# Kernel optimization log

Hardware: AMD Instinct MI355X
Metric: run time of the kernel (lower is better)

Reference implementation:

```python
import jax, jax.numpy as jnp
import numpy as np

B, M, L = 100, 100, 8
N = M * L
EPS = 1e-5  # torch BatchNorm2d default eps


def _conv(x, w, b, stride, pad):
    y = jax.lax.conv_general_dilated(x, w, (stride, stride), [(pad, pad), (pad, pad)],
                                     dimension_numbers=('NCHW', 'OIHW', 'NCHW'))
    return y + b[None, :, None, None]


def _convT(x, w, b, stride, pad):
    # torch ConvTranspose2d weight layout: (in_ch, out_ch, kH, kW)
    k = w.shape[2]
    wt = jnp.flip(w, (2, 3)).transpose(1, 0, 2, 3)  # -> OIHW
    p = k - 1 - pad
    y = jax.lax.conv_general_dilated(x, wt, (1, 1), [(p, p), (p, p)],
                                     lhs_dilation=(stride, stride),
                                     dimension_numbers=('NCHW', 'OIHW', 'NCHW'))
    return y + b[None, :, None, None]


def _bn(x):
    # BatchNorm2d constructed fresh in forward: weight=1, bias=0, batch stats (biased var)
    mean = x.mean(axis=(0, 2, 3), keepdims=True)
    var = x.var(axis=(0, 2, 3), keepdims=True)
    return (x - mean) / jnp.sqrt(var + EPS)


def _leaky(x):
    return jnp.where(x >= 0, x, 0.01 * x)


def _forward(x, conv1_w, conv1_b, conv2_w, conv2_b, conv3_w, conv3_b, conv4_w, conv4_b,
             fc_w, fc_b, dec_w, dec_b, ct1_w, ct1_b, ct2_w, ct2_b, ct3_w, ct3_b,
             ct4_w, ct4_b, ct5_w, ct5_b):
    # ---- encoder ----
    h = _bn(_leaky(_conv(x, conv1_w, conv1_b, 2, 1)))   # (B,128,32,32)
    h = _bn(_leaky(_conv(h, conv2_w, conv2_b, 2, 1)))   # (B,256,16,16)
    h = _bn(_leaky(_conv(h, conv3_w, conv3_b, 2, 1)))   # (B,1024,8,8)
    h = _bn(_leaky(_conv(h, conv4_w, conv4_b, 2, 1)))   # (B,1024,4,4)
    eig = jax.nn.relu(h.reshape(B, -1) @ fc_w + fc_b)   # (B, 800)
    # ---- latent_sample (training branch) ----
    sig = eig.reshape(B, M, L)
    row = jnp.sqrt(float(M * L)) * jnp.fft.ifft2(sig)          # complex (B,M,L)
    # original builds C via numpy/scipy per-sample -> detached; circulant[i,j] = c[(i-j) % n]
    row_flat = jax.lax.stop_gradient(row.real.reshape(B, N))
    i = jnp.arange(N)
    idx = (i[:, None] - i[None, :]) % N                        # (N,N) circulant gather
    C = row_flat[:, idx]                                       # (B,N,N)
    # original: Sigma_batch_eps[:, i] = eigenvalue (noise zeta is dead code), via numpy -> detached
    Y = jnp.fft.fft2(jax.lax.stop_gradient(sig)).real          # (B,M,L)
    # ---- decoder ----
    d = (Y.reshape(B, N) @ dec_w + dec_b).reshape(B, 1024, 3, 3)
    d = _convT(d, ct1_w, ct1_b, 2, 1)   # (B,512,5,5)
    d = _convT(d, ct2_w, ct2_b, 2, 0)   # (B,256,11,11)
    d = _convT(d, ct3_w, ct3_b, 2, 0)   # (B,128,23,23)
    d = _convT(d, ct4_w, ct4_b, 2, 0)   # (B,64,47,47)
    d = _convT(d, ct5_w, ct5_b, 1, 0)   # (B,1,49,49)
    return d, C, eig


def setup_inputs():
    key = jax.random.key(0)
    ks = jax.random.split(key, 16)

    def wv(k, shape, fan_in):
        return (jax.random.normal(k, shape, jnp.float32) / np.sqrt(fan_in)).astype(jnp.float32)

    return {
        'x': jax.random.normal(ks[0], (B, 1, 64, 64), jnp.float32),
        'conv1_w': wv(ks[1], (128, 1, 3, 3), 9), 'conv1_b': jnp.zeros((128,), jnp.float32),
        'conv2_w': wv(ks[2], (256, 128, 3, 3), 128 * 9), 'conv2_b': jnp.zeros((256,), jnp.float32),
        'conv3_w': wv(ks[3], (1024, 256, 3, 3), 256 * 9), 'conv3_b': jnp.zeros((1024,), jnp.float32),
        'conv4_w': wv(ks[4], (1024, 1024, 3, 3), 1024 * 9), 'conv4_b': jnp.zeros((1024,), jnp.float32),
        'fc_w': wv(ks[5], (1024 * 16, N), 1024 * 16), 'fc_b': jnp.zeros((N,), jnp.float32),
        'dec_w': wv(ks[6], (N, 1024 * 9), N), 'dec_b': jnp.zeros((1024 * 9,), jnp.float32),
        'ct1_w': wv(ks[7], (1024, 512, 3, 3), 1024 * 9), 'ct1_b': jnp.zeros((512,), jnp.float32),
        'ct2_w': wv(ks[8], (512, 256, 3, 3), 512 * 9), 'ct2_b': jnp.zeros((256,), jnp.float32),
        'ct3_w': wv(ks[9], (256, 128, 3, 3), 256 * 9), 'ct3_b': jnp.zeros((128,), jnp.float32),
        'ct4_w': wv(ks[10], (128, 64, 3, 3), 128 * 9), 'ct4_b': jnp.zeros((64,), jnp.float32),
        'ct5_w': wv(ks[11], (64, 1, 3, 3), 64 * 9), 'ct5_b': jnp.zeros((1,), jnp.float32),
    }


def reference(x, conv1_w, conv1_b, conv2_w, conv2_b, conv3_w, conv3_b, conv4_w, conv4_b,
              fc_w, fc_b, dec_w, dec_b, ct1_w, ct1_b, ct2_w, ct2_b, ct3_w, ct3_b,
              ct4_w, ct4_b, ct5_w, ct5_b):
    return _forward(x, conv1_w, conv1_b, conv2_w, conv2_b, conv3_w, conv3_b, conv4_w, conv4_b,
                    fc_w, fc_b, dec_w, dec_b, ct1_w, ct1_b, ct2_w, ct2_b, ct3_w, ct3_b,
                    ct4_w, ct4_b, ct5_w, ct5_b)
```

## Files before the change

kernel.cpp:

```cpp
#include <hip/hip_runtime.h>
#include <math.h>

typedef __attribute__((ext_vector_type(8))) short bf16x8;
typedef __attribute__((ext_vector_type(4))) float f32x4;
typedef unsigned short u16;

__device__ __forceinline__ u16 f2bf(float f) {
    unsigned u = __builtin_bit_cast(unsigned, f);
    u += 0x7FFFu + ((u >> 16) & 1u);
    return (u16)(u >> 16);
}
__device__ __forceinline__ float bf2f(u16 h) {
    unsigned u = ((unsigned)h) << 16;
    return __builtin_bit_cast(float, u);
}

template<int MODE, int OUT, int BM, int BN, int SWIZ, bool STATS>
__global__ __launch_bounds__(256, 3)
void gemm(const u16* __restrict__ Abf, const u16* __restrict__ Bw,
          const float* __restrict__ bias, void* __restrict__ outv,
          float* __restrict__ stat,
          int M, int N, int K, int lgC,
          int IH, int IW, int OH, int OW, int zchunk)
{
    constexpr int ANSEG = BM / 64, BNSEG = BN / 64;
    constexpr int RM = BM / 32, RN = BN / 32;
    __shared__ __align__(16) u16 As[4 * BM * 8];
    __shared__ __align__(16) u16 Bs[4 * BN * 8];
    const int t = threadIdx.x;
    const int lane = t & 63, wave = t >> 6;
    const int lm = lane & 15, quad = lane >> 4;
    const int wm = wave & 1, wn = wave >> 1;
    int mt, nt, z;
    if (SWIZ == 1) {
        int mtN = (M + BM - 1) / BM;
        int id = blockIdx.x;
        nt = id & 7; int j = id >> 3;
        mt = j % mtN; z = j / mtN;
    } else { mt = blockIdx.x; nt = blockIdx.y; z = blockIdx.z; }
    const int k0 = z * zchunk, kend = k0 + zchunk;

    const int arow = (ANSEG == 2) ? (t >> 1) : (t >> 2);
    const int akb  = (ANSEG == 2) ? (t & 1) * 16 : (t & 3) * 8;
    const int a_gm = mt * BM + arow;
    const bool a_in = a_gm < M;
    int oy = 0, ox = 0, bimg = 0;
    if (MODE == 1) {
        int ohw = OH * OW;
        int g = a_in ? a_gm : 0;
        bimg = g / ohw; int r = g - bimg * ohw;
        oy = r / OW; ox = r - (r / OW) * OW;
    }
    const int brow = (BNSEG == 2) ? (t >> 1) : (t >> 2);
    const int bkb  = (BNSEG == 2) ? (t & 1) * 16 : (t & 3) * 8;
    const int b_gn = nt * BN + brow;
    const bool b_in = b_gn < N;

    f32x4 acc[RM][RN];
    #pragma unroll
    for (int i = 0; i < RM; i++)
        #pragma unroll
        for (int j = 0; j < RN; j++) acc[i][j] = (f32x4){0.f, 0.f, 0.f, 0.f};

    for (int kb = k0; kb < kend; kb += 32) {
        #pragma unroll
        for (int s = 0; s < ANSEG; s++) {
            int kk = kb + akb + s * 8;
            uint4 v = make_uint4(0, 0, 0, 0);
            if (MODE == 0) {
                if (a_in) v = *(const uint4*)(Abf + (size_t)a_gm * K + kk);
            } else {
                int tap = kk >> lgC;
                int ic = kk & ((1 << lgC) - 1);
                int ky = tap / 3, kx = tap - (tap / 3) * 3;
                int iy = oy * 2 - 1 + ky, ix = ox * 2 - 1 + kx;
                if (a_in && (unsigned)iy < (unsigned)IH && (unsigned)ix < (unsigned)IW)
                    v = *(const uint4*)(Abf + ((((size_t)bimg * IH + iy) * IW + ix) << lgC) + ic);
            }
            *(uint4*)&As[(((akb >> 3) + s) * BM + arow) * 8] = v;
        }
        #pragma unroll
        for (int s = 0; s < BNSEG; s++) {
            int kk = kb + bkb + s * 8;
            uint4 v = make_uint4(0, 0, 0, 0);
            if (b_in) v = *(const uint4*)(Bw + (size_t)b_gn * K + kk);
            *(uint4*)&Bs[(((bkb >> 3) + s) * BN + brow) * 8] = v;
        }
        __syncthreads();
        bf16x8 af[RM], bfr[RN];
        #pragma unroll
        for (int i = 0; i < RM; i++)
            af[i] = *(const bf16x8*)&As[(size_t)(quad * BM + wm * (BM / 2) + i * 16 + lm) * 8];
        #pragma unroll
        for (int j = 0; j < RN; j++)
            bfr[j] = *(const bf16x8*)&Bs[(size_t)(quad * BN + wn * (BN / 2) + j * 16 + lm) * 8];
        #pragma unroll
        for (int i = 0; i < RM; i++)
            #pragma unroll
            for (int j = 0; j < RN; j++)
                acc[i][j] = __builtin_amdgcn_mfma_f32_16x16x32_bf16(af[i], bfr[j], acc[i][j], 0, 0, 0);
        __syncthreads();
    }

    const int n_base = nt * BN + wn * (BN / 2);
    const int m_base = mt * BM + wm * (BM / 2);
    int nj[RN]; float bvj[RN];
    #pragma unroll
    for (int j = 0; j < RN; j++) {
        nj[j] = n_base + j * 16 + lm;
        bvj[j] = 0.f;
        if (nj[j] < N && OUT != 4) {
            if (OUT == 0 || OUT == 5) bvj[j] = bias[nj[j]];
            else if (z == 0) bvj[j] = bias[nj[j]];
        }
    }
    if constexpr (OUT == 4) {
        float* op = (float*)outv;
        #pragma unroll
        for (int i = 0; i < RM; i++)
            #pragma unroll
            for (int r = 0; r < 4; r++) {
                int m = m_base + i * 16 + quad * 4 + r;
                if (m >= M) continue;
                #pragma unroll
                for (int j = 0; j < RN; j++)
                    if (nj[j] < N) atomicAdd(&op[(size_t)m * N + nj[j]], acc[i][j][r]);
            }
    } else if constexpr (OUT == 5) {
        u16* op = (u16*)outv;
        #pragma unroll
        for (int j = 0; j < RN; j++) {
            if (nj[j] >= N) continue;
            int c = nj[j] / 9, hw = nj[j] - c * 9;
            #pragma unroll
            for (int i = 0; i < RM; i++)
                #pragma unroll
                for (int r = 0; r < 4; r++) {
                    int m = m_base + i * 16 + quad * 4 + r;
                    if (m >= M) continue;
                    op[((size_t)m * 9 + hw) * 1024 + c] = f2bf(acc[i][j][r] + bvj[j]);
                }
        }
    } else if constexpr (OUT == 0) {
        int ohw = OH * OW;
        float sj[RN], qj[RN];
        #pragma unroll
        for (int j = 0; j < RN; j++) { sj[j] = 0.f; qj[j] = 0.f; }
        #pragma unroll
        for (int i = 0; i < RM; i++) {
            int m0 = m_base + i * 16 + quad * 4;
            if (m0 >= M) continue;
            int b = m0 / ohw, pix = m0 - b * ohw;
            #pragma unroll
            for (int j = 0; j < RN; j++) {
                if (nj[j] >= N) continue;
                #pragma unroll
                for (int r = 0; r < 4; r++) {
                    float val = acc[i][j][r] + bvj[j];
                    ((u16*)outv)[((size_t)b * ohw + pix + r) * N + nj[j]] = f2bf(val);
                    if (STATS) {
                        float lv = val >= 0.f ? val : 0.01f * val;
                        sj[j] += lv; qj[j] += lv * lv;
                    }
                }
            }
        }
        if constexpr (STATS) {
            #pragma unroll
            for (int j = 0; j < RN; j++) {
                float s = sj[j], q = qj[j];
                s += __shfl_down(s, 32); q += __shfl_down(q, 32);
                s += __shfl_down(s, 16); q += __shfl_down(q, 16);
                if (quad == 0 && nj[j] < N) {
                    atomicAdd(&stat[nj[j]], s);
                    atomicAdd(&stat[N + nj[j]], q);
                }
            }
        }
    } else {
        int ohw = OH * OW;
        #pragma unroll
        for (int i = 0; i < RM; i++) {
            int m0 = m_base + i * 16 + quad * 4;
            if (m0 >= M) continue;
            int b = m0 / ohw, pix = m0 - b * ohw;
            #pragma unroll
            for (int j = 0; j < RN; j++) {
                if (nj[j] >= N) continue;
                #pragma unroll
                for (int r = 0; r < 4; r++)
                    atomicAdd(&((float*)outv)[((size_t)b * ohw + pix + r) * N + nj[j]],
                              acc[i][j][r] + bvj[j]);
            }
        }
    }
}

template<int BM>
__global__ __launch_bounds__(256, 3)
void gemm_ct(const u16* __restrict__ Abf, const u16* __restrict__ Wb,
             const float* __restrict__ bias, u16* __restrict__ out,
             int N, int lgC, int IH, int IW, int OH, int OW,
             int4 Kc, int4 Mc, int4 Hc, int4 Wc, int4 Oc, int4 Dy, int4 Dx)
{
    constexpr int ANSEG = BM / 64;
    constexpr int RM = BM / 32, RN = 2;
    const int c = blockIdx.z;
    const int Ks[4] = {Kc.x, Kc.y, Kc.z, Kc.w};
    const int Ms[4] = {Mc.x, Mc.y, Mc.z, Mc.w};
    const int Hs[4] = {Hc.x, Hc.y, Hc.z, Hc.w};
    const int Wsz[4]= {Wc.x, Wc.y, Wc.z, Wc.w};
    const int Os[4] = {Oc.x, Oc.y, Oc.z, Oc.w};
    const int Dys[4]= {Dy.x, Dy.y, Dy.z, Dy.w};
    const int Dxs[4]= {Dx.x, Dx.y, Dx.z, Dx.w};
    const int K = Ks[c], M = Ms[c], OHc = Hs[c], OWc = Wsz[c];
    const int dyp = Dys[c], dxp = Dxs[c];
    const int mt = blockIdx.x, nt = blockIdx.y;
    if (mt * BM >= M) return;
    const u16* Bw = Wb + Os[c];

    __shared__ __align__(16) u16 As[4 * BM * 8];
    __shared__ __align__(16) u16 Bs[4 * 64 * 8];
    const int t = threadIdx.x;
    const int lane = t & 63, wave = t >> 6;
    const int lm = lane & 15, quad = lane >> 4;
    const int wm = wave & 1, wn = wave >> 1;

    const int arow = (ANSEG == 2) ? (t >> 1) : (t >> 2);
    const int akb  = (ANSEG == 2) ? (t & 1) * 16 : (t & 3) * 8;
    const int a_gm = mt * BM + arow;
    const bool a_in = a_gm < M;
    const int ohwc = OHc * OWc;
    int g = a_in ? a_gm : 0;
    int bimg = g / ohwc; int rr = g - bimg * ohwc;
    int oy = rr / OWc, ox = rr - (rr / OWc) * OWc;

    const int brow = t >> 2;
    const int bkb  = (t & 3) * 8;
    const int b_gn = nt * 64 + brow;
    const bool b_in = b_gn < N;

    f32x4 acc[RM][RN];
    #pragma unroll
    for (int i = 0; i < RM; i++)
        #pragma unroll
        for (int j = 0; j < RN; j++) acc[i][j] = (f32x4){0.f, 0.f, 0.f, 0.f};

    for (int kb = 0; kb < K; kb += 32) {
        #pragma unroll
        for (int s = 0; s < ANSEG; s++) {
            int kk = kb + akb + s * 8;
            uint4 v = make_uint4(0, 0, 0, 0);
            int ti = kk >> lgC;
            int ic = kk & ((1 << lgC) - 1);
            int dy = (int)(signed char)((dyp >> (8 * ti)) & 255);
            int dx = (int)(signed char)((dxp >> (8 * ti)) & 255);
            int iy = oy + dy, ix = ox + dx;
            if (a_in && (unsigned)iy < (unsigned)IH && (unsigned)ix < (unsigned)IW)
                v = *(const uint4*)(Abf + ((((size_t)bimg * IH + iy) * IW + ix) << lgC) + ic);
            *(uint4*)&As[(((akb >> 3) + s) * BM + arow) * 8] = v;
        }
        {
            uint4 v = make_uint4(0, 0, 0, 0);
            if (b_in) v = *(const uint4*)(Bw + (size_t)b_gn * K + kb + bkb);
            *(uint4*)&Bs[((bkb >> 3) * 64 + brow) * 8] = v;
        }
        __syncthreads();
        bf16x8 af[RM], bfr[RN];
        #pragma unroll
        for (int i = 0; i < RM; i++)
            af[i] = *(const bf16x8*)&As[(size_t)(quad * BM + wm * (BM / 2) + i * 16 + lm) * 8];
        #pragma unroll
        for (int j = 0; j < RN; j++)
            bfr[j] = *(const bf16x8*)&Bs[(size_t)(quad * 64 + wn * 32 + j * 16 + lm) * 8];
        #pragma unroll
        for (int i = 0; i < RM; i++)
            #pragma unroll
            for (int j = 0; j < RN; j++)
                acc[i][j] = __builtin_amdgcn_mfma_f32_16x16x32_bf16(af[i], bfr[j], acc[i][j], 0, 0, 0);
        __syncthreads();
    }

    const int n_base = nt * 64 + wn * 32;
    const int m_base = mt * BM + wm * (BM / 2);
    const int cy = c >> 1, cx = c & 1;
    const int OHW = OH * OW;
    int nj[RN]; float bvj[RN];
    #pragma unroll
    for (int j = 0; j < RN; j++) {
        nj[j] = n_base + j * 16 + lm;
        bvj[j] = (nj[j] < N) ? bias[nj[j]] : 0.f;
    }
    #pragma unroll
    for (int i = 0; i < RM; i++)
        #pragma unroll
        for (int r = 0; r < 4; r++) {
            int m = m_base + i * 16 + quad * 4 + r;
            if (m >= M) continue;
            int b = m / ohwc, r2 = m - b * ohwc;
            int oyc = r2 / OWc, oxc = r2 - (r2 / OWc) * OWc;
            size_t ad0 = ((size_t)b * OHW + (2 * oyc + cy) * OW + 2 * oxc + cx) * N;
            #pragma unroll
            for (int j = 0; j < RN; j++)
                if (nj[j] < N) out[ad0 + nj[j]] = f2bf(acc[i][j][r] + bvj[j]);
        }
}

__global__ __launch_bounds__(256)
void convw_prep(const float* __restrict__ src, u16* __restrict__ dst, int lgC, int total) {
    int idx = blockIdx.x * 256 + threadIdx.x;
    if (idx >= total) return;
    int K = 9 << lgC;
    int oc = idx / K, kk = idx - oc * K;
    int tap = kk >> lgC, ic = kk & ((1 << lgC) - 1);
    dst[idx] = f2bf(src[(((size_t)oc << lgC) + ic) * 9 + tap]);
}

__global__ __launch_bounds__(256)
void transpose_cvt(const float* __restrict__ in, u16* __restrict__ out, int R, int C) {
    __shared__ float tl[32][33];
    int c0 = blockIdx.x * 32, r0 = blockIdx.y * 32;
    int tx = threadIdx.x & 31, ty = threadIdx.x >> 5;
    #pragma unroll
    for (int l = 0; l < 4; l++)
        tl[ty + 8 * l][tx] = in[(size_t)(r0 + ty + 8 * l) * C + c0 + tx];
    __syncthreads();
    #pragma unroll
    for (int l = 0; l < 4; l++)
        out[(size_t)(c0 + ty + 8 * l) * R + r0 + tx] = f2bf(tl[tx][ty + 8 * l]);
}

__global__ __launch_bounds__(256)
void ctw_gather(const u16* __restrict__ tmp, u16* __restrict__ outw,
                int CIN, int lgC, int OC, int P) {
    int idx = blockIdx.x * 256 + threadIdx.x;
    if (idx >= (OC << lgC)) return;
    int ic = idx & (CIN - 1);
    int oc = idx >> lgC;
    int off = 0;
    for (int c = 0; c < 4; c++) {
        int cyP = (c >> 1) + P, cxP = (c & 1) + P;
        int nky = ((cyP & 1) == 0) ? 2 : 1;
        int nkx = ((cxP & 1) == 0) ? 2 : 1;
        int T = nky * nkx;
        int ti = 0;
        for (int ky = 0; ky < 3; ky++) {
            if ((cyP + ky) & 1) continue;
            for (int kx = 0; kx < 3; kx++) {
                if ((cxP + kx) & 1) continue;
                outw[off + (size_t)oc * (CIN * T) + ti * CIN + ic] =
                    tmp[((size_t)oc * 9 + ky * 3 + kx) * CIN + ic];
                ti++;
            }
        }
        off += OC * CIN * T;
    }
}

__global__ __launch_bounds__(256)
void fcw_prep(const float* __restrict__ in, u16* __restrict__ out) {
    __shared__ float tl[32][33];
    int n0 = blockIdx.x * 32, c0 = blockIdx.y * 32, hw = blockIdx.z;
    int tx = threadIdx.x & 31, ty = threadIdx.x >> 5;
    #pragma unroll
    for (int l = 0; l < 4; l++)
        tl[ty + 8 * l][tx] = in[((size_t)(c0 + ty + 8 * l) * 16 + hw) * 800 + n0 + tx];
    __syncthreads();
    #pragma unroll
    for (int l = 0; l < 4; l++)
        out[(size_t)(n0 + ty + 8 * l) * 16384 + hw * 1024 + c0 + tx] = f2bf(tl[tx][ty + 8 * l]);
}

__global__ __launch_bounds__(256)
void wt5_prep(const float* __restrict__ in, u16* __restrict__ out) {
    int idx = blockIdx.x * 256 + threadIdx.x;
    if (idx >= 576) return;
    int tap = idx >> 6, ic = idx & 63;
    out[idx] = f2bf(in[ic * 9 + tap]);
}

__global__ __launch_bounds__(256)
void conv1_nhwc(const float* __restrict__ x, const float* __restrict__ w,
                const float* __restrict__ bias, u16* __restrict__ out) {
    int idx = blockIdx.x * 256 + threadIdx.x;
    if (idx >= 100 * 1024 * 128) return;
    int oc = idx & 127;
    int pix = (idx >> 7) & 1023;
    int b = idx >> 17;
    int oy = pix >> 5, ox = pix & 31;
    int iy0 = oy * 2 - 1, ix0 = ox * 2 - 1;
    float acc = bias[oc];
    const float* ip = x + (size_t)b * 4096;
    const float* wp = w + oc * 9;
    #pragma unroll
    for (int ky = 0; ky < 3; ky++) {
        int iy = iy0 + ky;
        if ((unsigned)iy >= 64u) continue;
        #pragma unroll
        for (int kx = 0; kx < 3; kx++) {
            int ix = ix0 + kx;
            if ((unsigned)ix >= 64u) continue;
            acc = fmaf(ip[iy * 64 + ix], wp[ky * 3 + kx], acc);
        }
    }
    out[idx] = f2bf(acc);
}

template<typename T>
__global__ __launch_bounds__(256)
void bnstat(const T* __restrict__ x, float* __restrict__ accum, int C, int total) {
    int idx0 = blockIdx.x * 256 + threadIdx.x;
    int stride = gridDim.x * 256;
    float s = 0.f, q = 0.f;
    for (int i = idx0; i < total; i += stride) {
        float v;
        if constexpr (sizeof(T) == 2) v = bf2f(x[i]); else v = x[i];
        v = v >= 0.f ? v : 0.01f * v;
        s += v; q += v * v;
    }
    int c = idx0 & (C - 1);
    atomicAdd(&accum[c], s);
    atomicAdd(&accum[C + c], q);
}

template<typename T>
__global__ __launch_bounds__(256)
void bnapply(const T* __restrict__ x, u16* __restrict__ out,
             const float* __restrict__ accum, int C, int total, float invcnt) {
    int idx = blockIdx.x * 256 + threadIdx.x;
    if (idx >= total) return;
    int c = idx & (C - 1);
    float mean = accum[c] * invcnt;
    float var = accum[C + c] * invcnt - mean * mean;
    float inv = rsqrtf(var + 1e-5f);
    float v;
    if constexpr (sizeof(T) == 2) v = bf2f(x[idx]); else v = x[idx];
    v = v >= 0.f ? v : 0.01f * v;
    out[idx] = f2bf((v - mean) * inv);
}

__global__ __launch_bounds__(256)
void finalize_relu(const float* __restrict__ acc, const float* __restrict__ bias,
                   float* __restrict__ out) {
    int i = blockIdx.x * 256 + threadIdx.x;
    if (i >= 100 * 800) return;
    float v = acc[i] + bias[i % 800];
    out[i] = fmaxf(v, 0.f);
}

__global__ __launch_bounds__(256)
void dft_real(const float* __restrict__ eig, float* __restrict__ Yr, u16* __restrict__ Yrb) {
    __shared__ float se[800];
    __shared__ float ctab[800];
    int b = blockIdx.x;
    for (int i = threadIdx.x; i < 800; i += 256) {
        se[i] = eig[b * 800 + i];
        ctab[i] = (float)cos(6.283185307179586 * (double)i / 800.0);
    }
    __syncthreads();
    for (int oi = threadIdx.x; oi < 800; oi += 256) {
        int k1 = oi >> 3, k2 = oi & 7;
        int d1 = k1 * 8, d2 = k2 * 100;
        float acc = 0.f;
        int p1 = 0;
        for (int n1 = 0; n1 < 100; n1++) {
            int p = p1;
            #pragma unroll
            for (int n2 = 0; n2 < 8; n2++) {
                acc = fmaf(se[n1 * 8 + n2], ctab[p], acc);
                p += d2; if (p >= 800) p -= 800;
            }
            p1 += d1; if (p1 >= 800) p1 -= 800;
        }
        Yr[b * 800 + oi] = acc;
        Yrb[b * 800 + oi] = f2bf(acc);
    }
}

__global__ __launch_bounds__(256)
void build_C4(const float* __restrict__ Yr, float* __restrict__ C) {
    int idx = blockIdx.x * 256 + threadIdx.x;
    if (idx >= 100 * 800 * 200) return;
    int j4 = (idx % 200) * 4; int tt = idx / 200;
    int i = tt % 800;         int b = tt / 800;
    const float* y = Yr + b * 800;
    f32x4 v;
    #pragma unroll
    for (int r = 0; r < 4; r++) {
        int k = i - (j4 + r);
        k += (k >> 31) & 800;
        v[r] = y[k] * 0.035355339059327376f;
    }
    ((f32x4*)C)[idx] = v;
}

__global__ __launch_bounds__(256)
void convT5(const u16* __restrict__ in, const u16* __restrict__ w,
            const float* __restrict__ bias, float* __restrict__ out) {
    int idx = blockIdx.x * 256 + threadIdx.x;
    if (idx >= 100 * 49 * 49) return;
    int ox = idx % 49; int t2 = idx / 49;
    int oy = t2 % 49;  int b = t2 / 49;
    float acc = bias[0];
    for (int ky = 0; ky < 3; ky++) {
        int iy = oy - ky;
        if ((unsigned)iy >= 47u) continue;
        for (int kx = 0; kx < 3; kx++) {
            int ix = ox - kx;
            if ((unsigned)ix >= 47u) continue;
            const uint4* ip = (const uint4*)(in + (((size_t)b * 47 + iy) * 47 + ix) * 64);
            const uint4* wp = (const uint4*)(w + (ky * 3 + kx) * 64);
            #pragma unroll
            for (int g = 0; g < 8; g++) {
                uint4 av = ip[g], wv = wp[g];
                const unsigned* aa = (const unsigned*)&av;
                const unsigned* ww = (const unsigned*)&wv;
                #pragma unroll
                for (int h = 0; h < 4; h++) {
                    float a0 = __builtin_bit_cast(float, aa[h] << 16);
                    float a1 = __builtin_bit_cast(float, aa[h] & 0xFFFF0000u);
                    float w0 = __builtin_bit_cast(float, ww[h] << 16);
                    float w1 = __builtin_bit_cast(float, ww[h] & 0xFFFF0000u);
                    acc = fmaf(a0, w0, acc);
                    acc = fmaf(a1, w1, acc);
                }
            }
        }
    }
    out[idx] = acc;
}

struct CTClass { int T, OHc, OWc, dyp, dxp, off, K; };
static void ct_params(int P, int OH, int OW, int CIN, int OC, CTClass cls[4]) {
    int off = 0;
    for (int c = 0; c < 4; c++) {
        int cy = c >> 1, cx = c & 1;
        int kys[2], dys[2], nky = 0, kxs[2], dxs[2], nkx = 0;
        for (int ky = 0; ky < 3; ky++)
            if (((cy + P + ky) & 1) == 0) { kys[nky] = ky; dys[nky] = (cy + P - ky) / 2; nky++; }
        for (int kx = 0; kx < 3; kx++)
            if (((cx + P + kx) & 1) == 0) { kxs[nkx] = kx; dxs[nkx] = (cx + P - kx) / 2; nkx++; }
        CTClass& cc = cls[c];
        cc.T = nky * nkx;
        cc.OHc = (OH - cy + 1) >> 1; cc.OWc = (OW - cx + 1) >> 1;
        cc.dyp = 0; cc.dxp = 0;
        int ti = 0;
        for (int a = 0; a < nky; a++)
            for (int b2 = 0; b2 < nkx; b2++, ti++) {
                cc.dyp |= (dys[a] & 255) << (8 * ti);
                cc.dxp |= (dxs[b2] & 255) << (8 * ti);
            }
        cc.off = off; cc.K = CIN * cc.T;
        off += OC * cc.K;
    }
}

template<int BM>
static void launch_ct(hipStream_t s, const u16* in, const u16* W, const float* bias, u16* outp,
                      int lgC, int OC, int IH, int IW, int OH, int OW, const CTClass* cls) {
    int maxMT = 0;
    for (int c = 0; c < 4; c++) {
        int mt = (100 * cls[c].OHc * cls[c].OWc + BM - 1) / BM;
        if (mt > maxMT) maxMT = mt;
    }
    dim3 g(maxMT, (OC + 63) / 64, 4);
    gemm_ct<BM><<<g, 256, 0, s>>>(in, W, bias, outp, OC, lgC, IH, IW, OH, OW,
        make_int4(cls[0].K, cls[1].K, cls[2].K, cls[3].K),
        make_int4(100*cls[0].OHc*cls[0].OWc, 100*cls[1].OHc*cls[1].OWc,
                  100*cls[2].OHc*cls[2].OWc, 100*cls[3].OHc*cls[3].OWc),
        make_int4(cls[0].OHc, cls[1].OHc, cls[2].OHc, cls[3].OHc),
        make_int4(cls[0].OWc, cls[1].OWc, cls[2].OWc, cls[3].OWc),
        make_int4(cls[0].off, cls[1].off, cls[2].off, cls[3].off),
        make_int4(cls[0].dyp, cls[1].dyp, cls[2].dyp, cls[3].dyp),
        make_int4(cls[0].dxp, cls[1].dxp, cls[2].dxp, cls[3].dxp));
}

extern "C" void kernel_launch(void* const* d_in, const int* in_sizes, int n_in,
                              void* d_out, int out_size, void* d_ws, size_t ws_size,
                              hipStream_t stream) {
    const float* x    = (const float*)d_in[0];
    const float* c1w  = (const float*)d_in[1];  const float* c1b = (const float*)d_in[2];
    const float* c2w  = (const float*)d_in[3];  const float* c2b = (const float*)d_in[4];
    const float* c3w  = (const float*)d_in[5];  const float* c3b = (const float*)d_in[6];
    const float* c4w  = (const float*)d_in[7];  const float* c4b = (const float*)d_in[8];
    const float* fcw  = (const float*)d_in[9];  const float* fcb = (const float*)d_in[10];
    const float* decw = (const float*)d_in[11]; const float* decb = (const float*)d_in[12];
    const float* t1w  = (const float*)d_in[13]; const float* t1b = (const float*)d_in[14];
    const float* t2w  = (const float*)d_in[15]; const float* t2b = (const float*)d_in[16];
    const float* t3w  = (const float*)d_in[17]; const float* t3b = (const float*)d_in[18];
    const float* t4w  = (const float*)d_in[19]; const float* t4b = (const float*)d_in[20];
    const float* t5w  = (const float*)d_in[21]; const float* t5b = (const float*)d_in[22];

    float* out = (float*)d_out;
    float* d_final = out;
    float* Cmat    = out + 240100;
    float* eig     = out + 240100 + 64000000;

    float* ws = (float*)d_ws;
    u16*   h1    = (u16*)(ws);
    u16*   W_fc  = (u16*)(ws);
    u16*   h2    = (u16*)(ws + 6553600);
    u16*   h3    = (u16*)(ws + 9830400);
    u16*   W_c2  = (u16*)(ws + 13107200);
    u16*   W_c3  = (u16*)(ws + 13254656);
    u16*   W_c4  = (u16*)(ws + 14434304);
    float* h4f   = ws + 19152896;
    u16*   h4    = (u16*)(ws + 20791296);
    float* accs  = ws + 21610496;
    float* facc  = ws + 21618688;
    float* Yr    = ws + 21698688;
    u16*   Yrb   = (u16*)(ws + 21778688);
    u16*   d0    = (u16*)(ws + 21818688);
    u16*   W_dec = (u16*)(ws + 22279488);
    float* acc1 = accs, *acc2 = accs + 2048, *acc3 = accs + 4096, *acc4 = accs + 6144;
    u16*   W_t   = (u16*)(ws);
    u16*   tmpw  = (u16*)(ws + 2359296);
    u16*   o1    = (u16*)(ws + 4718592);
    u16*   o2    = (u16*)(ws + 5358592);
    u16*   o3    = (u16*)(ws + 6907392);
    u16*   o4    = (u16*)(ws + 10292992);
    u16*   W_t5  = (u16*)(ws + 17361792);

    #define GRID(n) dim3(((n) + 255) / 256)

    hipMemsetAsync(accs, 0, (8192 + 80000) * 4, stream);

    conv1_nhwc<<<GRID(13107200), 256, 0, stream>>>(x, c1w, c1b, h1);
    bnstat<u16><<<1024, 256, 0, stream>>>(h1, acc1, 128, 13107200);
    bnapply<u16><<<GRID(13107200), 256, 0, stream>>>(h1, h1, acc1, 128, 13107200, 1.f / 102400.f);

    convw_prep<<<GRID(294912), 256, 0, stream>>>(c2w, W_c2, 7, 294912);
    gemm<1, 0, 128, 128, 0, true><<<dim3(200, 2, 1), 256, 0, stream>>>(
        h1, W_c2, c2b, h2, acc2, 25600, 256, 1152, 7, 32, 32, 16, 16, 1152);
    bnapply<u16><<<GRID(6553600), 256, 0, stream>>>(h2, h2, acc2, 256, 6553600, 1.f / 25600.f);

    convw_prep<<<GRID(2359296), 256, 0, stream>>>(c3w, W_c3, 8, 2359296);
    gemm<1, 0, 128, 128, 1, true><<<dim3(400, 1, 1), 256, 0, stream>>>(
        h2, W_c3, c3b, h3, acc3, 6400, 1024, 2304, 8, 16, 16, 8, 8, 2304);
    bnapply<u16><<<GRID(6553600), 256, 0, stream>>>(h3, h3, acc3, 1024, 6553600, 1.f / 6400.f);

    convw_prep<<<GRID(9437184), 256, 0, stream>>>(c4w, W_c4, 10, 9437184);
    hipMemsetAsync(h4f, 0, 1638400 * 4, stream);
    gemm<1, 1, 64, 128, 1, false><<<dim3(400, 1, 1), 256, 0, stream>>>(
        h3, W_c4, c4b, h4f, nullptr, 1600, 1024, 9216, 10, 8, 8, 4, 4, 4608);
    bnstat<float><<<1024, 256, 0, stream>>>(h4f, acc4, 1024, 1638400);
    bnapply<float><<<GRID(1638400), 256, 0, stream>>>(h4f, h4, acc4, 1024, 1638400, 1.f / 1600.f);

    fcw_prep<<<dim3(25, 32, 16), 256, 0, stream>>>(fcw, W_fc);
    gemm<0, 4, 64, 64, 0, false><<<dim3(2, 13, 16), 256, 0, stream>>>(
        h4, W_fc, nullptr, facc, nullptr, 100, 800, 16384, 0, 0, 0, 0, 0, 1024);
    finalize_relu<<<GRID(80000), 256, 0, stream>>>(facc, fcb, eig);

    dft_real<<<dim3(100), 256, 0, stream>>>(eig, Yr, Yrb);
    build_C4<<<GRID(16000000), 256, 0, stream>>>(Yr, Cmat);

    transpose_cvt<<<dim3(288, 25), 256, 0, stream>>>(decw, W_dec, 800, 9216);
    gemm<0, 5, 64, 64, 0, false><<<dim3(2, 144, 1), 256, 0, stream>>>(
        Yrb, W_dec, decb, d0, nullptr, 100, 9216, 800, 0, 0, 0, 0, 0, 800);

    CTClass c1c[4], c2c[4], c3c[4], c4c[4];
    ct_params(1, 5, 5, 1024, 512, c1c);
    ct_params(0, 11, 11, 512, 256, c2c);
    ct_params(0, 23, 23, 256, 128, c3c);
    ct_params(0, 47, 47, 128, 64, c4c);

    transpose_cvt<<<dim3(144, 32), 256, 0, stream>>>(t1w, tmpw, 1024, 4608);
    ctw_gather<<<GRID(524288), 256, 0, stream>>>(tmpw, W_t, 1024, 10, 512, 1);
    launch_ct<64>(stream, d0, W_t, t1b, o1, 10, 512, 3, 3, 5, 5, c1c);

    transpose_cvt<<<dim3(72, 16), 256, 0, stream>>>(t2w, tmpw, 512, 2304);
    ctw_gather<<<GRID(131072), 256, 0, stream>>>(tmpw, W_t, 512, 9, 256, 0);
    launch_ct<64>(stream, o1, W_t, t2b, o2, 9, 256, 5, 5, 11, 11, c2c);

    transpose_cvt<<<dim3(36, 8), 256, 0, stream>>>(t3w, tmpw, 256, 1152);
    ctw_gather<<<GRID(32768), 256, 0, stream>>>(tmpw, W_t, 256, 8, 128, 0);
    launch_ct<64>(stream, o2, W_t, t3b, o3, 8, 128, 11, 11, 23, 23, c3c);

    transpose_cvt<<<dim3(18, 4), 256, 0, stream>>>(t4w, tmpw, 128, 576);
    ctw_gather<<<GRID(8192), 256, 0, stream>>>(tmpw, W_t, 128, 7, 64, 0);
    launch_ct<128>(stream, o3, W_t, t4b, o4, 7, 64, 23, 23, 47, 47, c4c);

    wt5_prep<<<GRID(576), 256, 0, stream>>>(t5w, W_t5);
    convT5<<<GRID(240100), 256, 0, stream>>>(o4, W_t5, t5b, d_final);

    #undef GRID
}
```

Baseline: 1.297 ms.

## Prefetch GEMM tiles, vectorize BatchNorm, fuse conv-transpose weight prep, split DFT

The GEMM and conv-transpose kernels now preload the next K-slice into registers while the current slice is computed, and replace per-iteration im2col index arithmetic with incrementally advanced pointers. The BatchNorm stat and apply kernels are rewritten to handle 8 bf16 or 4 fp32 values per thread, with per-block shared-memory reduction before the global atomics. The transpose and gather passes for conv-transpose weights are merged into one kernel. The DFT is split across two blocks per sample with two accumulators, and convT5 uses multiple partial accumulators. Register prefetch raises register pressure, and the changed summation orders alter rounding slightly.

Result: faster. 1.134 ms (-12.5%).

```diff
diff --git a/kernel.cpp b/kernel.cpp
--- a/kernel.cpp
+++ b/kernel.cpp
@@ -15,7 +15,7 @@
     return __builtin_bit_cast(float, u);
 }
 
-template<int MODE, int OUT, int BM, int BN, int SWIZ, bool STATS>
+template<int MODE, int OUT, int BM, int BN, int SWIZ, bool STATS, bool PF>
 __global__ __launch_bounds__(256, 3)
 void gemm(const u16* __restrict__ Abf, const u16* __restrict__ Bw,
           const float* __restrict__ bias, void* __restrict__ outv,
@@ -56,37 +56,75 @@
     const int b_gn = nt * BN + brow;
     const bool b_in = b_gn < N;
 
+    const int Cmask = (1 << lgC) - 1;
+    int ic_s = 0, tap_s = 0;
+    bool aok = a_in;
+    const u16* aptr;
+    if (MODE == 0) {
+        aptr = Abf + (size_t)a_gm * K + k0 + akb;
+    } else {
+        int kk0 = k0 + akb;
+        tap_s = kk0 >> lgC; ic_s = kk0 & Cmask;
+        int ky = tap_s / 3, kx = tap_s - (tap_s / 3) * 3;
+        int iy = oy * 2 - 1 + ky, ix = ox * 2 - 1 + kx;
+        aok = a_in && (unsigned)iy < (unsigned)IH && (unsigned)ix < (unsigned)IW;
+        aptr = Abf + ((((size_t)bimg * IH + iy) * IW + ix) << lgC);
+    }
+    const u16* bptr = Bw + (size_t)b_gn * K + k0 + bkb;
+
+    auto ldA = [&](uint4 (&v)[ANSEG]) {
+        #pragma unroll
+        for (int s = 0; s < ANSEG; s++) {
+            uint4 x4 = make_uint4(0, 0, 0, 0);
+            if (MODE == 0) {
+                if (aok) x4 = *(const uint4*)(aptr + s * 8);
+            } else {
+                if (aok) x4 = *(const uint4*)(aptr + ic_s + s * 8);
+            }
+            v[s] = x4;
+        }
+        if (MODE == 0) {
+            aptr += 32;
+        } else {
+            ic_s += 32;
+            if (ic_s > Cmask) {
+                ic_s -= Cmask + 1;
+                tap_s++;
+                int ky = tap_s / 3, kx = tap_s - (tap_s / 3) * 3;
+                int iy = oy * 2 - 1 + ky, ix = ox * 2 - 1 + kx;
+                aok = a_in && (unsigned)iy < (unsigned)IH && (unsigned)ix < (unsigned)IW;
+                aptr = Abf + ((((size_t)bimg * IH + iy) * IW + ix) << lgC);
+            }
+        }
+    };
+    auto ldB = [&](uint4 (&v)[BNSEG]) {
+        #pragma unroll
+        for (int s = 0; s < BNSEG; s++) {
+            uint4 x4 = make_uint4(0, 0, 0, 0);
+            if (b_in) x4 = *(const uint4*)(bptr + s * 8);
+            v[s] = x4;
+        }
+        bptr += 32;
+    };
+
     f32x4 acc[RM][RN];
     #pragma unroll
     for (int i = 0; i < RM; i++)
         #pragma unroll
         for (int j = 0; j < RN; j++) acc[i][j] = (f32x4){0.f, 0.f, 0.f, 0.f};
 
+    uint4 va[ANSEG], vb[BNSEG];
+    if (PF) { ldA(va); ldB(vb); }
     for (int kb = k0; kb < kend; kb += 32) {
-        #pragma unroll
-        for (int s = 0; s < ANSEG; s++) {
-            int kk = kb + akb + s * 8;
-            uint4 v = make_uint4(0, 0, 0, 0);
-            if (MODE == 0) {
-                if (a_in) v = *(const uint4*)(Abf + (size_t)a_gm * K + kk);
-            } else {
-                int tap = kk >> lgC;
-                int ic = kk & ((1 << lgC) - 1);
-                int ky = tap / 3, kx = tap - (tap / 3) * 3;
-                int iy = oy * 2 - 1 + ky, ix = ox * 2 - 1 + kx;
-                if (a_in && (unsigned)iy < (unsigned)IH && (unsigned)ix < (unsigned)IW)
-                    v = *(const uint4*)(Abf + ((((size_t)bimg * IH + iy) * IW + ix) << lgC) + ic);
-            }
-            *(uint4*)&As[(((akb >> 3) + s) * BM + arow) * 8] = v;
-        }
-        #pragma unroll
-        for (int s = 0; s < BNSEG; s++) {
-            int kk = kb + bkb + s * 8;
-            uint4 v = make_uint4(0, 0, 0, 0);
-            if (b_in) v = *(const uint4*)(Bw + (size_t)b_gn * K + kk);
-            *(uint4*)&Bs[(((bkb >> 3) + s) * BN + brow) * 8] = v;
-        }
+        if (!PF) { ldA(va); ldB(vb); }
+        #pragma unroll
+        for (int s = 0; s < ANSEG; s++)
+            *(uint4*)&As[(((akb >> 3) + s) * BM + arow) * 8] = va[s];
+        #pragma unroll
+        for (int s = 0; s < BNSEG; s++)
+            *(uint4*)&Bs[(((bkb >> 3) + s) * BN + brow) * 8] = vb[s];
         __syncthreads();
+        if (PF && kb + 32 < kend) { ldA(va); ldB(vb); }
         bf16x8 af[RM], bfr[RN];
         #pragma unroll
         for (int i = 0; i < RM; i++)
@@ -240,32 +278,61 @@
     const int b_gn = nt * 64 + brow;
     const bool b_in = b_gn < N;
 
+    const int Cmask = (1 << lgC) - 1;
+    int ic_s = akb & Cmask;
+    int ti_s = 0;
+    bool aok; const u16* aptr;
+    {
+        int sh = 8 * (ti_s & 3);
+        int dy = (int)(signed char)((dyp >> sh) & 255);
+        int dx = (int)(signed char)((dxp >> sh) & 255);
+        int iy = oy + dy, ix = ox + dx;
+        aok = a_in && (unsigned)iy < (unsigned)IH && (unsigned)ix < (unsigned)IW;
+        aptr = Abf + ((((size_t)bimg * IH + iy) * IW + ix) << lgC);
+    }
+    const u16* bptr = Bw + (size_t)b_gn * K + bkb;
+
+    auto ldA = [&](uint4 (&v)[ANSEG]) {
+        #pragma unroll
+        for (int s = 0; s < ANSEG; s++) {
+            uint4 x4 = make_uint4(0, 0, 0, 0);
+            if (aok) x4 = *(const uint4*)(aptr + ic_s + s * 8);
+            v[s] = x4;
+        }
+        ic_s += 32;
+        if (ic_s > Cmask) {
+            ic_s -= Cmask + 1;
+            ti_s++;
+            int sh = 8 * (ti_s & 3);
+            int dy = (int)(signed char)((dyp >> sh) & 255);
+            int dx = (int)(signed char)((dxp >> sh) & 255);
+            int iy = oy + dy, ix = ox + dx;
+            aok = a_in && (unsigned)iy < (unsigned)IH && (unsigned)ix < (unsigned)IW;
+            aptr = Abf + ((((size_t)bimg * IH + iy) * IW + ix) << lgC);
+        }
+    };
+    auto ldB = [&](uint4& v) {
+        uint4 x4 = make_uint4(0, 0, 0, 0);
+        if (b_in) x4 = *(const uint4*)bptr;
+        v = x4;
+        bptr += 32;
+    };
+
     f32x4 acc[RM][RN];
     #pragma unroll
     for (int i = 0; i < RM; i++)
         #pragma unroll
         for (int j = 0; j < RN; j++) acc[i][j] = (f32x4){0.f, 0.f, 0.f, 0.f};
 
+    uint4 va[ANSEG]; uint4 vb;
+    ldA(va); ldB(vb);
     for (int kb = 0; kb < K; kb += 32) {
         #pragma unroll
-        for (int s = 0; s < ANSEG; s++) {
-            int kk = kb + akb + s * 8;
-            uint4 v = make_uint4(0, 0, 0, 0);
-            int ti = kk >> lgC;
-            int ic = kk & ((1 << lgC) - 1);
-            int dy = (int)(signed char)((dyp >> (8 * ti)) & 255);
-            int dx = (int)(signed char)((dxp >> (8 * ti)) & 255);
-            int iy = oy + dy, ix = ox + dx;
-            if (a_in && (unsigned)iy < (unsigned)IH && (unsigned)ix < (unsigned)IW)
-                v = *(const uint4*)(Abf + ((((size_t)bimg * IH + iy) * IW + ix) << lgC) + ic);
-            *(uint4*)&As[(((akb >> 3) + s) * BM + arow) * 8] = v;
-        }
-        {
-            uint4 v = make_uint4(0, 0, 0, 0);
-            if (b_in) v = *(const uint4*)(Bw + (size_t)b_gn * K + kb + bkb);
-            *(uint4*)&Bs[((bkb >> 3) * 64 + brow) * 8] = v;
-        }
+        for (int s = 0; s < ANSEG; s++)
+            *(uint4*)&As[(((akb >> 3) + s) * BM + arow) * 8] = va[s];
+        *(uint4*)&Bs[((bkb >> 3) * 64 + brow) * 8] = vb;
         __syncthreads();
+        if (kb + 32 < K) { ldA(va); ldB(vb); }
         bf16x8 af[RM], bfr[RN];
         #pragma unroll
         for (int i = 0; i < RM; i++)
@@ -331,29 +398,29 @@
 }
 
 __global__ __launch_bounds__(256)
-void ctw_gather(const u16* __restrict__ tmp, u16* __restrict__ outw,
-                int CIN, int lgC, int OC, int P) {
-    int idx = blockIdx.x * 256 + threadIdx.x;
-    if (idx >= (OC << lgC)) return;
-    int ic = idx & (CIN - 1);
-    int oc = idx >> lgC;
-    int off = 0;
-    for (int c = 0; c < 4; c++) {
-        int cyP = (c >> 1) + P, cxP = (c & 1) + P;
-        int nky = ((cyP & 1) == 0) ? 2 : 1;
-        int nkx = ((cxP & 1) == 0) ? 2 : 1;
-        int T = nky * nkx;
-        int ti = 0;
-        for (int ky = 0; ky < 3; ky++) {
-            if ((cyP + ky) & 1) continue;
-            for (int kx = 0; kx < 3; kx++) {
-                if ((cxP + kx) & 1) continue;
-                outw[off + (size_t)oc * (CIN * T) + ti * CIN + ic] =
-                    tmp[((size_t)oc * 9 + ky * 3 + kx) * CIN + ic];
-                ti++;
-            }
-        }
-        off += OC * CIN * T;
+void ctw_fused(const float* __restrict__ in, u16* __restrict__ outw,
+               int CIN, int P, int4 Kc, int4 Oc) {
+    __shared__ float tl[32][33];
+    int c0 = blockIdx.x * 32, r0 = blockIdx.y * 32;
+    int C = gridDim.x * 32;
+    int tx = threadIdx.x & 31, ty = threadIdx.x >> 5;
+    #pragma unroll
+    for (int l = 0; l < 4; l++)
+        tl[ty + 8 * l][tx] = in[(size_t)(r0 + ty + 8 * l) * C + c0 + tx];
+    __syncthreads();
+    const int Ks[4] = {Kc.x, Kc.y, Kc.z, Kc.w};
+    const int Os[4] = {Oc.x, Oc.y, Oc.z, Oc.w};
+    int ic = r0 + tx;
+    #pragma unroll
+    for (int l = 0; l < 4; l++) {
+        int cc = c0 + ty + 8 * l;
+        int oc = cc / 9, tap = cc - 9 * oc;
+        int ky = tap / 3, kx = tap - 3 * (tap / 3);
+        int cyc = (P + ky) & 1, cxc = (P + kx) & 1;
+        int cls = cyc * 2 + cxc;
+        int nkx = ((P ^ cxc) & 1) ? 1 : 2;
+        int ti = (ky >> 1) * nkx + (kx >> 1);
+        outw[Os[cls] + (size_t)oc * Ks[cls] + ti * CIN + ic] = f2bf(tl[tx][ty + 8 * l]);
     }
 }
 
@@ -406,37 +473,109 @@
     out[idx] = f2bf(acc);
 }
 
-template<typename T>
-__global__ __launch_bounds__(256)
-void bnstat(const T* __restrict__ x, float* __restrict__ accum, int C, int total) {
-    int idx0 = blockIdx.x * 256 + threadIdx.x;
-    int stride = gridDim.x * 256;
-    float s = 0.f, q = 0.f;
-    for (int i = idx0; i < total; i += stride) {
-        float v;
-        if constexpr (sizeof(T) == 2) v = bf2f(x[i]); else v = x[i];
-        v = v >= 0.f ? v : 0.01f * v;
-        s += v; q += v * v;
-    }
-    int c = idx0 & (C - 1);
-    atomicAdd(&accum[c], s);
-    atomicAdd(&accum[C + c], q);
-}
-
-template<typename T>
-__global__ __launch_bounds__(256)
-void bnapply(const T* __restrict__ x, u16* __restrict__ out,
-             const float* __restrict__ accum, int C, int total, float invcnt) {
-    int idx = blockIdx.x * 256 + threadIdx.x;
-    if (idx >= total) return;
-    int c = idx & (C - 1);
-    float mean = accum[c] * invcnt;
-    float var = accum[C + c] * invcnt - mean * mean;
-    float inv = rsqrtf(var + 1e-5f);
-    float v;
-    if constexpr (sizeof(T) == 2) v = bf2f(x[idx]); else v = x[idx];
-    v = v >= 0.f ? v : 0.01f * v;
-    out[idx] = f2bf((v - mean) * inv);
+__global__ __launch_bounds__(256)
+void bnstat8(const u16* __restrict__ x, float* __restrict__ accum, int C, int total) {
+    __shared__ float ls[2048];
+    for (int i = threadIdx.x; i < 2 * C; i += 256) ls[i] = 0.f;
+    __syncthreads();
+    int base = (blockIdx.x * 256 + threadIdx.x) * 8;
+    int stride = gridDim.x * 256 * 8;
+    float s[8], q[8];
+    #pragma unroll
+    for (int r = 0; r < 8; r++) { s[r] = 0.f; q[r] = 0.f; }
+    for (int i = base; i < total; i += stride) {
+        uint4 v = *(const uint4*)(x + i);
+        const unsigned* w = (const unsigned*)&v;
+        #pragma unroll
+        for (int h = 0; h < 4; h++) {
+            float v0 = __builtin_bit_cast(float, w[h] << 16);
+            float v1 = __builtin_bit_cast(float, w[h] & 0xFFFF0000u);
+            v0 = v0 >= 0.f ? v0 : 0.01f * v0;
+            v1 = v1 >= 0.f ? v1 : 0.01f * v1;
+            s[2 * h] += v0;     q[2 * h] += v0 * v0;
+            s[2 * h + 1] += v1; q[2 * h + 1] += v1 * v1;
+        }
+    }
+    int c0 = base & (C - 1);
+    #pragma unroll
+    for (int r = 0; r < 8; r++) {
+        atomicAdd(&ls[c0 + r], s[r]);
+        atomicAdd(&ls[C + c0 + r], q[r]);
+    }
+    __syncthreads();
+    for (int i = threadIdx.x; i < 2 * C; i += 256) atomicAdd(&accum[i], ls[i]);
+}
+
+__global__ __launch_bounds__(256)
+void bnapply8(const u16* __restrict__ x, u16* __restrict__ out,
+              const float* __restrict__ accum, int C, int total, float invcnt) {
+    int i8 = (blockIdx.x * 256 + threadIdx.x) * 8;
+    if (i8 >= total) return;
+    int c0 = i8 & (C - 1);
+    uint4 v = *(const uint4*)(x + i8);
+    const unsigned* w = (const unsigned*)&v;
+    uint4 o;
+    unsigned* ow = (unsigned*)&o;
+    #pragma unroll
+    for (int h = 0; h < 4; h++) {
+        float m0 = accum[c0 + 2 * h] * invcnt, m1 = accum[c0 + 2 * h + 1] * invcnt;
+        float q0 = accum[C + c0 + 2 * h] * invcnt, q1 = accum[C + c0 + 2 * h + 1] * invcnt;
+        float in0 = rsqrtf(q0 - m0 * m0 + 1e-5f);
+        float in1 = rsqrtf(q1 - m1 * m1 + 1e-5f);
+        float v0 = __builtin_bit_cast(float, w[h] << 16);
+        float v1 = __builtin_bit_cast(float, w[h] & 0xFFFF0000u);
+        v0 = v0 >= 0.f ? v0 : 0.01f * v0;
+        v1 = v1 >= 0.f ? v1 : 0.01f * v1;
+        unsigned r0 = f2bf((v0 - m0) * in0);
+        unsigned r1 = f2bf((v1 - m1) * in1);
+        ow[h] = r0 | (r1 << 16);
+    }
+    *(uint4*)(out + i8) = o;
+}
+
+__global__ __launch_bounds__(256)
+void bnstat4f(const float* __restrict__ x, float* __restrict__ accum, int C, int total) {
+    __shared__ float ls[2048];
+    for (int i = threadIdx.x; i < 2 * C; i += 256) ls[i] = 0.f;
+    __syncthreads();
+    int base = (blockIdx.x * 256 + threadIdx.x) * 4;
+    int stride = gridDim.x * 1024;
+    float s[4] = {0, 0, 0, 0}, q[4] = {0, 0, 0, 0};
+    for (int i = base; i < total; i += stride) {
+        f32x4 v = *(const f32x4*)(x + i);
+        #pragma unroll
+        for (int r = 0; r < 4; r++) {
+            float vv = v[r]; vv = vv >= 0.f ? vv : 0.01f * vv;
+            s[r] += vv; q[r] += vv * vv;
+        }
+    }
+    int c0 = base & (C - 1);
+    #pragma unroll
+    for (int r = 0; r < 4; r++) {
+        atomicAdd(&ls[c0 + r], s[r]);
+        atomicAdd(&ls[C + c0 + r], q[r]);
+    }
+    __syncthreads();
+    for (int i = threadIdx.x; i < 2 * C; i += 256) atomicAdd(&accum[i], ls[i]);
+}
+
+__global__ __launch_bounds__(256)
+void bnapply4f(const float* __restrict__ x, u16* __restrict__ out,
+               const float* __restrict__ accum, int C, int total, float invcnt) {
+    int i4 = (blockIdx.x * 256 + threadIdx.x) * 4;
+    if (i4 >= total) return;
+    int c0 = i4 & (C - 1);
+    f32x4 v = *(const f32x4*)(x + i4);
+    unsigned r4[4];
+    #pragma unroll
+    for (int r = 0; r < 4; r++) {
+        float m = accum[c0 + r] * invcnt;
+        float var = accum[C + c0 + r] * invcnt - m * m;
+        float inv = rsqrtf(var + 1e-5f);
+        float vv = v[r]; vv = vv >= 0.f ? vv : 0.01f * vv;
+        r4[r] = f2bf((vv - m) * inv);
+    }
+    *(uint2*)(out + i4) = make_uint2(r4[0] | (r4[1] << 16), r4[2] | (r4[3] << 16));
 }
 
 __global__ __launch_bounds__(256)
@@ -455,23 +594,32 @@
     int b = blockIdx.x;
     for (int i = threadIdx.x; i < 800; i += 256) {
         se[i] = eig[b * 800 + i];
-        ctab[i] = (float)cos(6.283185307179586 * (double)i / 800.0);
+        ctab[i] = cospif(i * 0.0025f);
     }
     __syncthreads();
-    for (int oi = threadIdx.x; oi < 800; oi += 256) {
+    int o0 = blockIdx.y * 400;
+    for (int oi = o0 + threadIdx.x; oi < o0 + 400; oi += 256) {
         int k1 = oi >> 3, k2 = oi & 7;
         int d1 = k1 * 8, d2 = k2 * 100;
-        float acc = 0.f;
+        float acc0 = 0.f, acc1 = 0.f;
         int p1 = 0;
-        for (int n1 = 0; n1 < 100; n1++) {
+        for (int n1 = 0; n1 < 100; n1 += 2) {
             int p = p1;
             #pragma unroll
             for (int n2 = 0; n2 < 8; n2++) {
-                acc = fmaf(se[n1 * 8 + n2], ctab[p], acc);
+                acc0 = fmaf(se[n1 * 8 + n2], ctab[p], acc0);
                 p += d2; if (p >= 800) p -= 800;
             }
-            p1 += d1; if (p1 >= 800) p1 -= 800;
-        }
+            int pb = p1 + d1; if (pb >= 800) pb -= 800;
+            int p2 = pb;
+            #pragma unroll
+            for (int n2 = 0; n2 < 8; n2++) {
+                acc1 = fmaf(se[(n1 + 1) * 8 + n2], ctab[p2], acc1);
+                p2 += d2; if (p2 >= 800) p2 -= 800;
+            }
+            p1 = pb + d1; if (p1 >= 800) p1 -= 800;
+        }
+        float acc = acc0 + acc1;
         Yr[b * 800 + oi] = acc;
         Yrb[b * 800 + oi] = f2bf(acc);
     }
@@ -501,7 +649,9 @@
     if (idx >= 100 * 49 * 49) return;
     int ox = idx % 49; int t2 = idx / 49;
     int oy = t2 % 49;  int b = t2 / 49;
-    float acc = bias[0];
+    float ac[8];
+    #pragma unroll
+    for (int r = 0; r < 8; r++) ac[r] = 0.f;
     for (int ky = 0; ky < 3; ky++) {
         int iy = oy - ky;
         if ((unsigned)iy >= 47u) continue;
@@ -521,13 +671,15 @@
                     float a1 = __builtin_bit_cast(float, aa[h] & 0xFFFF0000u);
                     float w0 = __builtin_bit_cast(float, ww[h] << 16);
                     float w1 = __builtin_bit_cast(float, ww[h] & 0xFFFF0000u);
-                    acc = fmaf(a0, w0, acc);
-                    acc = fmaf(a1, w1, acc);
+                    int rix = ((g & 1) << 2) | h;
+                    ac[rix] = fmaf(a0, w0, ac[rix]);
+                    ac[rix] = fmaf(a1, w1, ac[rix]);
                 }
             }
         }
     }
-    out[idx] = acc;
+    out[idx] = bias[0] + ((ac[0] + ac[1]) + (ac[2] + ac[3]))
+                       + ((ac[4] + ac[5]) + (ac[6] + ac[7]));
 }
 
 struct CTClass { int T, OHc, OWc, dyp, dxp, off, K; };
@@ -575,6 +727,14 @@
         make_int4(cls[0].dxp, cls[1].dxp, cls[2].dxp, cls[3].dxp));
 }
 
+static void launch_ctw(hipStream_t s, const float* w, u16* outw,
+                       int CIN, int OC, int P, const CTClass* cls) {
+    dim3 g((OC * 9) / 32, CIN / 32);
+    ctw_fused<<<g, 256, 0, s>>>(w, outw, CIN, P,
+        make_int4(cls[0].K, cls[1].K, cls[2].K, cls[3].K),
+        make_int4(cls[0].off, cls[1].off, cls[2].off, cls[3].off));
+}
+
 extern "C" void kernel_launch(void* const* d_in, const int* in_sizes, int n_in,
                               void* d_out, int out_size, void* d_ws, size_t ws_size,
                               hipStream_t stream) {
@@ -614,7 +774,6 @@
     u16*   W_dec = (u16*)(ws + 22279488);
     float* acc1 = accs, *acc2 = accs + 2048, *acc3 = accs + 4096, *acc4 = accs + 6144;
     u16*   W_t   = (u16*)(ws);
-    u16*   tmpw  = (u16*)(ws + 2359296);
     u16*   o1    = (u16*)(ws + 4718592);
     u16*   o2    = (u16*)(ws + 5358592);
     u16*   o3    = (u16*)(ws + 6907392);
@@ -626,36 +785,36 @@
     hipMemsetAsync(accs, 0, (8192 + 80000) * 4, stream);
 
     conv1_nhwc<<<GRID(13107200), 256, 0, stream>>>(x, c1w, c1b, h1);
-    bnstat<u16><<<1024, 256, 0, stream>>>(h1, acc1, 128, 13107200);
-    bnapply<u16><<<GRID(13107200), 256, 0, stream>>>(h1, h1, acc1, 128, 13107200, 1.f / 102400.f);
+    bnstat8<<<1024, 256, 0, stream>>>(h1, acc1, 128, 13107200);
+    bnapply8<<<GRID(1638400), 256, 0, stream>>>(h1, h1, acc1, 128, 13107200, 1.f / 102400.f);
 
     convw_prep<<<GRID(294912), 256, 0, stream>>>(c2w, W_c2, 7, 294912);
-    gemm<1, 0, 128, 128, 0, true><<<dim3(200, 2, 1), 256, 0, stream>>>(
+    gemm<1, 0, 128, 128, 0, true, false><<<dim3(200, 2, 1), 256, 0, stream>>>(
         h1, W_c2, c2b, h2, acc2, 25600, 256, 1152, 7, 32, 32, 16, 16, 1152);
-    bnapply<u16><<<GRID(6553600), 256, 0, stream>>>(h2, h2, acc2, 256, 6553600, 1.f / 25600.f);
+    bnapply8<<<GRID(819200), 256, 0, stream>>>(h2, h2, acc2, 256, 6553600, 1.f / 25600.f);
 
     convw_prep<<<GRID(2359296), 256, 0, stream>>>(c3w, W_c3, 8, 2359296);
-    gemm<1, 0, 128, 128, 1, true><<<dim3(400, 1, 1), 256, 0, stream>>>(
+    gemm<1, 0, 128, 128, 1, true, false><<<dim3(400, 1, 1), 256, 0, stream>>>(
         h2, W_c3, c3b, h3, acc3, 6400, 1024, 2304, 8, 16, 16, 8, 8, 2304);
-    bnapply<u16><<<GRID(6553600), 256, 0, stream>>>(h3, h3, acc3, 1024, 6553600, 1.f / 6400.f);
+    bnapply8<<<GRID(819200), 256, 0, stream>>>(h3, h3, acc3, 1024, 6553600, 1.f / 6400.f);
 
     convw_prep<<<GRID(9437184), 256, 0, stream>>>(c4w, W_c4, 10, 9437184);
     hipMemsetAsync(h4f, 0, 1638400 * 4, stream);
-    gemm<1, 1, 64, 128, 1, false><<<dim3(400, 1, 1), 256, 0, stream>>>(
+    gemm<1, 1, 64, 128, 1, false, true><<<dim3(400, 1, 1), 256, 0, stream>>>(
         h3, W_c4, c4b, h4f, nullptr, 1600, 1024, 9216, 10, 8, 8, 4, 4, 4608);
-    bnstat<float><<<1024, 256, 0, stream>>>(h4f, acc4, 1024, 1638400);
-    bnapply<float><<<GRID(1638400), 256, 0, stream>>>(h4f, h4, acc4, 1024, 1638400, 1.f / 1600.f);
+    bnstat4f<<<1024, 256, 0, stream>>>(h4f, acc4, 1024, 1638400);
+    bnapply4f<<<GRID(409600), 256, 0, stream>>>(h4f, h4, acc4, 1024, 1638400, 1.f / 1600.f);
 
     fcw_prep<<<dim3(25, 32, 16), 256, 0, stream>>>(fcw, W_fc);
-    gemm<0, 4, 64, 64, 0, false><<<dim3(2, 13, 16), 256, 0, stream>>>(
+    gemm<0, 4, 64, 64, 0, false, true><<<dim3(2, 13, 16), 256, 0, stream>>>(
         h4, W_fc, nullptr, facc, nullptr, 100, 800, 16384, 0, 0, 0, 0, 0, 1024);
     finalize_relu<<<GRID(80000), 256, 0, stream>>>(facc, fcb, eig);
 
-    dft_real<<<dim3(100), 256, 0, stream>>>(eig, Yr, Yrb);
+    dft_real<<<dim3(100, 2), 256, 0, stream>>>(eig, Yr, Yrb);
     build_C4<<<GRID(16000000), 256, 0, stream>>>(Yr, Cmat);
 
     transpose_cvt<<<dim3(288, 25), 256, 0, stream>>>(decw, W_dec, 800, 9216);
-    gemm<0, 5, 64, 64, 0, false><<<dim3(2, 144, 1), 256, 0, stream>>>(
+    gemm<0, 5, 64, 64, 0, false, true><<<dim3(2, 144, 1), 256, 0, stream>>>(
         Yrb, W_dec, decb, d0, nullptr, 100, 9216, 800, 0, 0, 0, 0, 0, 800);
 
     CTClass c1c[4], c2c[4], c3c[4], c4c[4];
@@ -664,20 +823,16 @@
     ct_params(0, 23, 23, 256, 128, c3c);
     ct_params(0, 47, 47, 128, 64, c4c);
 
-    transpose_cvt<<<dim3(144, 32), 256, 0, stream>>>(t1w, tmpw, 1024, 4608);
-    ctw_gather<<<GRID(524288), 256, 0, stream>>>(tmpw, W_t, 1024, 10, 512, 1);
+    launch_ctw(stream, t1w, W_t, 1024, 512, 1, c1c);
     launch_ct<64>(stream, d0, W_t, t1b, o1, 10, 512, 3, 3, 5, 5, c1c);
 
-    transpose_cvt<<<dim3(72, 16), 256, 0, stream>>>(t2w, tmpw, 512, 2304);
-    ctw_gather<<<GRID(131072), 256, 0, stream>>>(tmpw, W_t, 512, 9, 256, 0);
+    launch_ctw(stream, t2w, W_t, 512, 256, 0, c2c);
     launch_ct<64>(stream, o1, W_t, t2b, o2, 9, 256, 5, 5, 11, 11, c2c);
 
-    transpose_cvt<<<dim3(36, 8), 256, 0, stream>>>(t3w, tmpw, 256, 1152);
-    ctw_gather<<<GRID(32768), 256, 0, stream>>>(tmpw, W_t, 256, 8, 128, 0);
+    launch_ctw(stream, t3w, W_t, 256, 128, 0, c3c);
     launch_ct<64>(stream, o2, W_t, t3b, o3, 8, 128, 11, 11, 23, 23, c3c);
 
-    transpose_cvt<<<dim3(18, 4), 256, 0, stream>>>(t4w, tmpw, 128, 576);
-    ctw_gather<<<GRID(8192), 256, 0, stream>>>(tmpw, W_t, 128, 7, 64, 0);
+    launch_ctw(stream, t4w, W_t, 128, 64, 0, c4c);
     launch_ct<128>(stream, o3, W_t, t4b, o4, 7, 64, 23, 23, 47, 47, c4c);
 
     wt5_prep<<<GRID(576), 256, 0, stream>>>(t5w, W_t5);
```
